# Optimization experiments

Measured on AMD Instinct MI355X. Metric: run time of the kernel, lower is better.

## Reference

```python
import jax, jax.numpy as jnp
import numpy as np

B, S, D = 2, 2048, 1024
E, K = 8, 2
H = 4 * D  # mlp_ratio = 4


def setup_inputs() -> dict:
    key = jax.random.key(0)
    ks = jax.random.split(key, 7)
    s_in = 1.0 / np.sqrt(D)
    s_hid = 1.0 / np.sqrt(H)
    return {
        "x": jax.random.normal(ks[0], (B, S, D), dtype=jnp.float32),
        "w1": jax.random.uniform(ks[1], (E, D, H), jnp.float32, -s_in, s_in),
        "b1": jax.random.uniform(ks[2], (E, H), jnp.float32, -s_in, s_in),
        "w2": jax.random.uniform(ks[3], (E, H, D), jnp.float32, -s_hid, s_hid),
        "b2": jax.random.uniform(ks[4], (E, D), jnp.float32, -s_hid, s_hid),
        "gate_w": jax.random.uniform(ks[5], (D, E), jnp.float32, -s_in, s_in),
        "gate_b": jax.random.uniform(ks[6], (E,), jnp.float32, -s_in, s_in),
    }


def reference(x, w1, b1, w2, b2, gate_w, gate_b):
    # Gating: top-k over expert logits, softmax over the selected k scores.
    scores = jnp.einsum("bsd,de->bse", x, gate_w) + gate_b          # [B,S,E]
    topk_scores, topk_idx = jax.lax.top_k(scores, K)                 # [B,S,K]
    probs = jax.nn.softmax(topk_scores, axis=-1)                     # [B,S,K]

    # Dense per-expert MLP on all tokens (faithful to the original's math).
    h = jnp.einsum("bsd,edh->bseh", x, w1) + b1                      # [B,S,E,H]
    h = jax.nn.gelu(h, approximate=False)                            # torch nn.GELU is exact erf
    y = jnp.einsum("bseh,ehd->bsed", h, w2) + b2                     # [B,S,E,D]

    # Select the top-k expert outputs and combine with softmax weights.
    sel = jnp.take_along_axis(y, topk_idx[..., None], axis=2)        # [B,S,K,D]
    out = jnp.einsum("bsk,bskd->bsd", probs, sel)                    # [B,S,D]
    return out
```

## Files before the change

### kernel.cpp

```cpp
#include <hip/hip_runtime.h>
#include <hip/hip_bf16.h>
#include <stdint.h>

#define D_DIM 1024
#define H_DIM 4096
#define E_NUM 8
#define NTOK  4096
#define CAP_E 4096
#define BM 128
#define BN 128
#define BK 64

typedef __bf16 bf16x8 __attribute__((ext_vector_type(8)));
typedef float  f32x4  __attribute__((ext_vector_type(4)));

static __device__ __forceinline__ unsigned short f2bf(float f) {
    union { float f; unsigned u; } v; v.f = f;
    unsigned r = v.u + 0x7fffu + ((v.u >> 16) & 1u);
    return (unsigned short)(r >> 16);
}

static __device__ __forceinline__ void gload16(const unsigned short* g, unsigned short* l) {
    __builtin_amdgcn_global_load_lds(
        (const __attribute__((address_space(1))) unsigned int*)g,
        (__attribute__((address_space(3))) unsigned int*)l,
        16, 0, 0);
}

static __device__ __forceinline__ float gelu_f(float v) {
    const float z = fabsf(v) * 0.70710678118654752f;
    const float t = __builtin_amdgcn_rcpf(__builtin_fmaf(0.3275911f, z, 1.f));
    float p = __builtin_fmaf(1.061405429f, t, -1.453152027f);
    p = __builtin_fmaf(p, t, 1.421413741f);
    p = __builtin_fmaf(p, t, -0.284496736f);
    p = __builtin_fmaf(p, t, 0.254829592f);
    const float e = 1.f - p * t * __expf(-z * z);
    const float erfv = (v < 0.f) ? -e : e;
    return v * (0.5f + 0.5f * erfv);
}

__global__ __launch_bounds__(256) void gate_kernel(
    const float* __restrict__ x, const float* __restrict__ gw,
    const float* __restrict__ gb, int* __restrict__ counts,
    int* __restrict__ tok_list, float* __restrict__ prob_list,
    unsigned short* __restrict__ xb)
{
    const int wave = threadIdx.x >> 6, lane = threadIdx.x & 63;
    const int t = blockIdx.x * 4 + wave;
    double s[E_NUM];
#pragma unroll
    for (int j = 0; j < E_NUM; ++j) s[j] = 0.0;
    const float* xr = x + (size_t)t * D_DIM;
    unsigned short* xbr = xb + (size_t)t * D_DIM;
#pragma unroll
    for (int i = 0; i < D_DIM / 64; ++i) {
        const int d = i * 64 + lane;
        const float xv = xr[d];
        xbr[d] = f2bf(xv);
        const float4 g0 = *(const float4*)(gw + d * 8);
        const float4 g1 = *(const float4*)(gw + d * 8 + 4);
        s[0] += (double)xv * g0.x; s[1] += (double)xv * g0.y;
        s[2] += (double)xv * g0.z; s[3] += (double)xv * g0.w;
        s[4] += (double)xv * g1.x; s[5] += (double)xv * g1.y;
        s[6] += (double)xv * g1.z; s[7] += (double)xv * g1.w;
    }
#pragma unroll
    for (int off = 32; off >= 1; off >>= 1)
#pragma unroll
        for (int j = 0; j < E_NUM; ++j) s[j] += __shfl_xor(s[j], off, 64);

    if (lane == 0) {
#pragma unroll
        for (int j = 0; j < E_NUM; ++j) s[j] += (double)gb[j];
        int i0 = 0;
        for (int j = 1; j < E_NUM; ++j) if (s[j] > s[i0]) i0 = j;
        int i1 = (i0 == 0) ? 1 : 0;
        for (int j = 0; j < E_NUM; ++j) if (j != i0 && s[j] > s[i1]) i1 = j;
        const double e1 = exp(s[i1] - s[i0]);
        const float p0 = (float)(1.0 / (1.0 + e1));
        const float p1 = (float)(e1 / (1.0 + e1));
        int pos0 = atomicAdd(&counts[i0], 1);
        tok_list[i0 * CAP_E + pos0]  = t;
        prob_list[i0 * CAP_E + pos0] = p0;
        int pos1 = atomicAdd(&counts[i1], 1);
        tok_list[i1 * CAP_E + pos1]  = t;
        prob_list[i1 * CAP_E + pos1] = p1;
    }
}

__global__ void offsets_kernel(const int* __restrict__ counts, int* __restrict__ offsets) {
    if (threadIdx.x == 0) {
        int acc = 0;
        for (int e = 0; e < E_NUM; ++e) { offsets[e] = acc; acc += counts[e]; }
    }
}

__global__ __launch_bounds__(256) void wtrans_kernel(
    const float* __restrict__ in, unsigned short* __restrict__ out, int R, int C)
{
    __shared__ unsigned tile[64][33];
    const size_t slab = (size_t)blockIdx.z * (size_t)R * C;
    const float* inp = in + slab;
    unsigned short* outp = out + slab;
    const int c0 = blockIdx.x * 64, r0 = blockIdx.y * 64;
    const int tid = threadIdx.x;
    const int cq = tid & 15, p0 = tid >> 4;
#pragma unroll
    for (int s = 0; s < 2; ++s) {
        const int p = p0 + s * 16;
        const int r = r0 + 2 * p;
        const int c = c0 + cq * 4;
        const float4 va = *(const float4*)(inp + (size_t)r * C + c);
        const float4 vb = *(const float4*)(inp + (size_t)(r + 1) * C + c);
        const float* fa = (const float*)&va;
        const float* fb = (const float*)&vb;
#pragma unroll
        for (int i = 0; i < 4; ++i)
            tile[cq * 4 + i][p] = (unsigned)f2bf(fa[i]) | ((unsigned)f2bf(fb[i]) << 16);
    }
    __syncthreads();
    const int cl = tid >> 2, q = tid & 3;
#pragma unroll
    for (int s = 0; s < 2; ++s) {
        const int qq = q + s * 4;
        uint4 wv;
        wv.x = tile[cl][qq * 4 + 0]; wv.y = tile[cl][qq * 4 + 1];
        wv.z = tile[cl][qq * 4 + 2]; wv.w = tile[cl][qq * 4 + 3];
        *(uint4*)(outp + (size_t)(c0 + cl) * R + r0 + qq * 8) = wv;
    }
}

__global__ __launch_bounds__(256) void expert_fc1(
    const unsigned short* __restrict__ xb, const unsigned short* __restrict__ w1t,
    const float* __restrict__ b1, const int* __restrict__ counts,
    const int* __restrict__ offsets, const int* __restrict__ tok_list,
    unsigned short* __restrict__ h_ws,
    int e_param, int we_param, int row_start, int cap, int packed)
{
    __shared__ __align__(16) unsigned short smem[12288];
    unsigned short* As = smem;
    unsigned short* Bs = smem + 4096;

    int e, bx, by;
    if (e_param >= 0) { e = e_param; bx = (int)blockIdx.x & 31; by = (int)blockIdx.x >> 5; }
    else { e = (int)blockIdx.x & 7; const int r = (int)blockIdx.x >> 3; bx = r & 31; by = r >> 5; }

    const int we = (we_param >= 0) ? we_param : e;
    const int cnt = counts[e];
    const int row_end = min(cnt, row_start + cap);
    const int row0 = row_start + by * 64;
    if (row0 >= row_end) return;
    const int n0 = bx * BN;
    const int hb = packed ? offsets[e] : 0;
    const int tid = threadIdx.x;

    const int wv = tid >> 6, lane = tid & 63;
    const int schunk = (lane & 7) ^ (lane >> 3);
    const unsigned short* __restrict__ w1e = w1t + (size_t)we * H_DIM * D_DIM;

    const unsigned short* aptr[2];
#pragma unroll
    for (int j = 0; j < 2; ++j) {
        const int rloc = (wv * 2 + j) * 8 + (lane >> 3);
        const int rr = min(row0 + rloc, row_end - 1);
        aptr[j] = xb + (size_t)tok_list[e * CAP_E + rr] * D_DIM + schunk * 8;
    }
    const unsigned short* bptr[4];
#pragma unroll
    for (int j = 0; j < 4; ++j) {
        const int rloc = (wv * 4 + j) * 8 + (lane >> 3);
        bptr[j] = w1e + (size_t)(n0 + rloc) * D_DIM + schunk * 8;
    }

    const int wc = wv * 32;
    const int rl = lane & 15, x7 = lane & 7, kg = lane >> 4;
    int aoff[2][4], boff[2][2];
#pragma unroll
    for (int s = 0; s < 2; ++s) {
        const int slot = ((((s << 2) + kg) ^ x7) << 3);
#pragma unroll
        for (int m = 0; m < 4; ++m) aoff[s][m] = ((m * 16 + rl) << 6) + slot;
#pragma unroll
        for (int n = 0; n < 2; ++n) boff[s][n] = ((wc + n * 16 + rl) << 6) + slot;
    }

    f32x4 acc[4][2];
#pragma unroll
    for (int m = 0; m < 4; ++m)
#pragma unroll
        for (int n = 0; n < 2; ++n) acc[m][n] = (f32x4){0.f, 0.f, 0.f, 0.f};

    for (int kk = 0; kk < D_DIM; kk += BK) {
        __syncthreads();
#pragma unroll
        for (int j = 0; j < 2; ++j)
            gload16(aptr[j] + kk, &As[(wv * 2 + j) * 512]);
#pragma unroll
        for (int j = 0; j < 4; ++j)
            gload16(bptr[j] + kk, &Bs[(wv * 4 + j) * 512]);
        __syncthreads();
#pragma unroll
        for (int s = 0; s < 2; ++s) {
            bf16x8 af[4], bfv[2];
#pragma unroll
            for (int m = 0; m < 4; ++m) af[m] = *(const bf16x8*)&As[aoff[s][m]];
#pragma unroll
            for (int n = 0; n < 2; ++n) bfv[n] = *(const bf16x8*)&Bs[boff[s][n]];
#pragma unroll
            for (int m = 0; m < 4; ++m)
#pragma unroll
                for (int n = 0; n < 2; ++n)
                    acc[m][n] = __builtin_amdgcn_mfma_f32_16x16x32_bf16(af[m], bfv[n], acc[m][n], 0, 0, 0);
        }
    }

    const float* __restrict__ b1e = b1 + e * H_DIM;
    const int crb = (lane >> 4) * 4, ccol = lane & 15;
    float bias[2];
#pragma unroll
    for (int n = 0; n < 2; ++n) bias[n] = b1e[n0 + wc + n * 16 + ccol];

    __syncthreads();
#pragma unroll
    for (int n = 0; n < 2; ++n)
#pragma unroll
        for (int m = 0; m < 4; ++m)
#pragma unroll
            for (int j = 0; j < 4; ++j) {
                const int rloc = m * 16 + crb + j;
                const int col = wc + n * 16 + ccol;
                smem[rloc * 132 + col] = f2bf(gelu_f(acc[m][n][j] + bias[n]));
            }
    __syncthreads();
#pragma unroll
    for (int i = 0; i < 4; ++i) {
        const int idx = tid + i * 256;
        const int row = idx >> 4, c8 = idx & 15;
        const uint4 val = *(const uint4*)&smem[row * 132 + c8 * 8];
        const int gr = row0 + row;
        if (gr < row_end)
            *(uint4*)&h_ws[(size_t)(hb + gr - row_start) * H_DIM + n0 + c8 * 8] = val;
    }
}

__global__ __launch_bounds__(256) void expert_fc2(
    const unsigned short* __restrict__ h_ws, const unsigned short* __restrict__ w2t,
    const float* __restrict__ b2, const int* __restrict__ counts,
    const int* __restrict__ offsets, const int* __restrict__ tok_list,
    const float* __restrict__ prob_list, float* __restrict__ out,
    int splitk, int e_param, int we_param, int row_start, int cap, int packed)
{
    __shared__ __align__(16) unsigned short As[64 * BK];
    __shared__ __align__(16) unsigned short Bs[128 * BK];

    int e, bx, by, ks;
    if (e_param >= 0) { e = e_param; bx = (int)blockIdx.x & 7; by = (int)blockIdx.x >> 3; ks = 0; }
    else { bx = (int)blockIdx.x & 7; int r = (int)blockIdx.x >> 3;
           by = r & 63; r >>= 6; ks = r & 1; e = r >> 1; }

    const int we = (we_param >= 0) ? we_param : e;
    const int cnt = counts[e];
    const int row_end = min(cnt, row_start + cap);
    const int row0 = row_start + by * 64;
    if (row0 >= row_end) return;
    const int n0 = bx * BN;
    const int hb = packed ? offsets[e] : 0;
    const int tid = threadIdx.x;

    const int kspan = H_DIM / splitk;
    const int k0 = ks * kspan;

    const int wv = tid >> 6, lane = tid & 63;
    const int schunk = (lane & 7) ^ (lane >> 3);
    const unsigned short* __restrict__ w2e = w2t + (size_t)we * D_DIM * H_DIM;

    const unsigned short* aptr[2];
#pragma unroll
    for (int j = 0; j < 2; ++j) {
        const int rloc = (wv * 2 + j) * 8 + (lane >> 3);
        int r = row0 + rloc; if (r >= row_end) r = row_end - 1;
        aptr[j] = h_ws + (size_t)(hb + r - row_start) * H_DIM + k0 + schunk * 8;
    }
    const unsigned short* bptr[4];
#pragma unroll
    for (int j = 0; j < 4; ++j) {
        const int rloc = (wv * 4 + j) * 8 + (lane >> 3);
        bptr[j] = w2e + (size_t)(n0 + rloc) * H_DIM + k0 + schunk * 8;
    }

    const int wc = wv * 32;
    const int rl = lane & 15, x7 = lane & 7, kg = lane >> 4;
    int aoff[2][4], boff[2][2];
#pragma unroll
    for (int s = 0; s < 2; ++s) {
        const int slot = ((((s << 2) + kg) ^ x7) << 3);
#pragma unroll
        for (int m = 0; m < 4; ++m) aoff[s][m] = ((m * 16 + rl) << 6) + slot;
#pragma unroll
        for (int n = 0; n < 2; ++n) boff[s][n] = ((wc + n * 16 + rl) << 6) + slot;
    }

    f32x4 acc[4][2];
#pragma unroll
    for (int m = 0; m < 4; ++m)
#pragma unroll
        for (int n = 0; n < 2; ++n) acc[m][n] = (f32x4){0.f, 0.f, 0.f, 0.f};

    for (int kk = 0; kk < kspan; kk += BK) {
        __syncthreads();
#pragma unroll
        for (int j = 0; j < 2; ++j)
            gload16(aptr[j] + kk, &As[(wv * 2 + j) * 512]);
#pragma unroll
        for (int j = 0; j < 4; ++j)
            gload16(bptr[j] + kk, &Bs[(wv * 4 + j) * 512]);
        __syncthreads();
#pragma unroll
        for (int s = 0; s < 2; ++s) {
            bf16x8 af[4], bfv[2];
#pragma unroll
            for (int m = 0; m < 4; ++m) af[m] = *(const bf16x8*)&As[aoff[s][m]];
#pragma unroll
            for (int n = 0; n < 2; ++n) bfv[n] = *(const bf16x8*)&Bs[boff[s][n]];
#pragma unroll
            for (int m = 0; m < 4; ++m)
#pragma unroll
                for (int n = 0; n < 2; ++n)
                    acc[m][n] = __builtin_amdgcn_mfma_f32_16x16x32_bf16(af[m], bfv[n], acc[m][n], 0, 0, 0);
        }
    }

    const float* __restrict__ b2e = b2 + e * D_DIM;
    const int crb = (lane >> 4) * 4, ccol = lane & 15;
#pragma unroll
    for (int n = 0; n < 2; ++n) {
        const int gc = n0 + wc + n * 16 + ccol;
        const float bias = (ks == 0) ? b2e[gc] : 0.f;
#pragma unroll
        for (int m = 0; m < 4; ++m) {
#pragma unroll
            for (int j = 0; j < 4; ++j) {
                const int gr = row0 + m * 16 + crb + j;
                if (gr < row_end) {
                    const float yv = acc[m][n][j] + bias;
                    const int t = tok_list[e * CAP_E + gr];
                    const float p = prob_list[e * CAP_E + gr];
                    atomicAdd(&out[(size_t)t * D_DIM + gc], p * yv);
                }
            }
        }
    }
}

extern "C" void kernel_launch(void* const* d_in, const int* in_sizes, int n_in,
                              void* d_out, int out_size, void* d_ws, size_t ws_size,
                              hipStream_t stream)
{
    const float* x  = (const float*)d_in[0];
    const float* w1 = (const float*)d_in[1];
    const float* b1 = (const float*)d_in[2];
    const float* w2 = (const float*)d_in[3];
    const float* b2 = (const float*)d_in[4];
    const float* gw = (const float*)d_in[5];
    const float* gb = (const float*)d_in[6];
    float* out = (float*)d_out;

    char* w = (char*)d_ws;
    int*   counts    = (int*)w;
    int*   offsets   = (int*)(w + 64);
    int*   tok_list  = (int*)(w + 128);
    float* prob_list = (float*)(w + 128 + (size_t)CAP_E * E_NUM * 4);
    size_t off = 128 + 2 * (size_t)CAP_E * E_NUM * 4;
    off = (off + 255) & ~(size_t)255;
    unsigned short* xb = (unsigned short*)(w + off);
    off += (size_t)NTOK * D_DIM * 2;

    const size_t wslab = (size_t)D_DIM * H_DIM * 2;
    const size_t hfull = (size_t)2 * NTOK * H_DIM * 2;
    const size_t need_full = off + 2 * E_NUM * wslab + hfull;

    hipMemsetAsync(d_out, 0, (size_t)out_size * sizeof(float), stream);
    hipMemsetAsync(counts, 0, 64, stream);

    gate_kernel<<<NTOK / 4, 256, 0, stream>>>(x, gw, gb, counts, tok_list, prob_list, xb);
    offsets_kernel<<<1, 64, 0, stream>>>(counts, offsets);

    if (ws_size >= need_full) {
        unsigned short* w1t = (unsigned short*)(w + off);
        unsigned short* w2t = (unsigned short*)(w + off + E_NUM * wslab);
        unsigned short* h_ws = (unsigned short*)(w + off + 2 * E_NUM * wslab);

        wtrans_kernel<<<dim3(H_DIM / 64, D_DIM / 64, E_NUM), 256, 0, stream>>>(w1, w1t, D_DIM, H_DIM);
        wtrans_kernel<<<dim3(D_DIM / 64, H_DIM / 64, E_NUM), 256, 0, stream>>>(w2, w2t, H_DIM, D_DIM);

        expert_fc1<<<8 * 32 * 64, 256, 0, stream>>>(
            xb, w1t, b1, counts, offsets, tok_list, h_ws, -1, -1, 0, NTOK, 1);
        expert_fc2<<<8 * 64 * 2 * 8, 256, 0, stream>>>(
            h_ws, w2t, b2, counts, offsets, tok_list, prob_list, out,
            2, -1, -1, 0, NTOK, 1);
    } else {
        unsigned short* w1te = (unsigned short*)(w + off);
        unsigned short* w2te = (unsigned short*)(w + off + wslab);
        size_t h_off = off + 2 * wslab;
        unsigned short* h_e = (unsigned short*)(w + h_off);
        size_t h_avail = (ws_size > h_off) ? (ws_size - h_off) / ((size_t)H_DIM * 2) : 0;
        int cap = (int)((h_avail < (size_t)NTOK) ? h_avail : (size_t)NTOK);
        cap = (cap / BM) * BM;
        if (cap < BM) cap = BM;
        const int chunks = (NTOK + cap - 1) / cap;
        for (int e = 0; e < E_NUM; ++e) {
            wtrans_kernel<<<dim3(H_DIM / 64, D_DIM / 64, 1), 256, 0, stream>>>(
                w1 + (size_t)e * D_DIM * H_DIM, w1te, D_DIM, H_DIM);
            wtrans_kernel<<<dim3(D_DIM / 64, H_DIM / 64, 1), 256, 0, stream>>>(
                w2 + (size_t)e * H_DIM * D_DIM, w2te, H_DIM, D_DIM);
            for (int c = 0; c < chunks; ++c) {
                const int rs = c * cap;
                expert_fc1<<<32 * ((cap + 63) / 64), 256, 0, stream>>>(
                    xb, w1te, b1, counts, offsets, tok_list, h_e,
                    e, 0, rs, cap, 0);
                expert_fc2<<<8 * ((cap + 63) / 64), 256, 0, stream>>>(
                    h_e, w2te, b2, counts, offsets, tok_list, prob_list, out,
                    1, e, 0, rs, cap, 0);
            }
        }
    }
}
```

Before: 469.9 us.

## Fuse gate with w1 transpose and fc1 with w2 transpose into combined launches

Merges the gating kernel with the w1 fp32-to-bf16 transpose, and the fc1 GEMM with the w2 transpose, into two combined launches that split work by block index. The memory-bound transpose blocks can then overlap with compute-bound or latency-bound work, and two kernel launch boundaries and their tail effects go away. The cost is a shared LDS pool sized for the largest role, which may reduce occupancy for the transpose blocks, and blocks with mixed behaviour inside one grid.

After: 450.6 us. -4.1%, faster.

```diff
diff --git a/kernel.cpp b/kernel.cpp
--- a/kernel.cpp
+++ b/kernel.cpp
@@ -10,6 +10,11 @@
 #define BM 128
 #define BN 128
 #define BK 64
+
+#define GATE_BLKS (NTOK / 4)
+#define W1T_BLKS  (64 * 16 * E_NUM)
+#define FC1_BLKS  (E_NUM * 32 * 64)
+#define W2T_BLKS  (16 * 64 * E_NUM)
 
 typedef __bf16 bf16x8 __attribute__((ext_vector_type(8)));
 typedef float  f32x4  __attribute__((ext_vector_type(4)));
@@ -39,14 +44,15 @@
     return v * (0.5f + 0.5f * erfv);
 }
 
-__global__ __launch_bounds__(256) void gate_kernel(
+
+static __device__ void gate_body(
     const float* __restrict__ x, const float* __restrict__ gw,
     const float* __restrict__ gb, int* __restrict__ counts,
     int* __restrict__ tok_list, float* __restrict__ prob_list,
-    unsigned short* __restrict__ xb)
+    unsigned short* __restrict__ xb, int bid)
 {
     const int wave = threadIdx.x >> 6, lane = threadIdx.x & 63;
-    const int t = blockIdx.x * 4 + wave;
+    const int t = bid * 4 + wave;
     double s[E_NUM];
 #pragma unroll
     for (int j = 0; j < E_NUM; ++j) s[j] = 0.0;
@@ -88,21 +94,15 @@
     }
 }
 
-__global__ void offsets_kernel(const int* __restrict__ counts, int* __restrict__ offsets) {
-    if (threadIdx.x == 0) {
-        int acc = 0;
-        for (int e = 0; e < E_NUM; ++e) { offsets[e] = acc; acc += counts[e]; }
-    }
-}
-
-__global__ __launch_bounds__(256) void wtrans_kernel(
-    const float* __restrict__ in, unsigned short* __restrict__ out, int R, int C)
-{
-    __shared__ unsigned tile[64][33];
-    const size_t slab = (size_t)blockIdx.z * (size_t)R * C;
+static __device__ void wtrans_body(
+    char* pool, const float* __restrict__ in, unsigned short* __restrict__ out,
+    int R, int C, int cx, int cy, int bz)
+{
+    unsigned (*tile)[33] = (unsigned (*)[33])pool;
+    const size_t slab = (size_t)bz * (size_t)R * C;
     const float* inp = in + slab;
     unsigned short* outp = out + slab;
-    const int c0 = blockIdx.x * 64, r0 = blockIdx.y * 64;
+    const int c0 = cx * 64, r0 = cy * 64;
     const int tid = threadIdx.x;
     const int cq = tid & 15, p0 = tid >> 4;
 #pragma unroll
@@ -130,22 +130,18 @@
     }
 }
 
-__global__ __launch_bounds__(256) void expert_fc1(
+static __device__ void fc1_body(
+    char* pool,
     const unsigned short* __restrict__ xb, const unsigned short* __restrict__ w1t,
     const float* __restrict__ b1, const int* __restrict__ counts,
     const int* __restrict__ offsets, const int* __restrict__ tok_list,
     unsigned short* __restrict__ h_ws,
-    int e_param, int we_param, int row_start, int cap, int packed)
-{
-    __shared__ __align__(16) unsigned short smem[12288];
+    int e, int we, int bx, int by, int row_start, int cap, int packed)
+{
+    unsigned short* smem = (unsigned short*)pool;
     unsigned short* As = smem;
     unsigned short* Bs = smem + 4096;
 
-    int e, bx, by;
-    if (e_param >= 0) { e = e_param; bx = (int)blockIdx.x & 31; by = (int)blockIdx.x >> 5; }
-    else { e = (int)blockIdx.x & 7; const int r = (int)blockIdx.x >> 3; bx = r & 31; by = r >> 5; }
-
-    const int we = (we_param >= 0) ? we_param : e;
     const int cnt = counts[e];
     const int row_end = min(cnt, row_start + cap);
     const int row0 = row_start + by * 64;
@@ -241,6 +237,83 @@
         if (gr < row_end)
             *(uint4*)&h_ws[(size_t)(hb + gr - row_start) * H_DIM + n0 + c8 * 8] = val;
     }
+}
+
+
+__global__ __launch_bounds__(256) void fused_gate_w1trans(
+    const float* __restrict__ x, const float* __restrict__ gw,
+    const float* __restrict__ gb, int* __restrict__ counts,
+    int* __restrict__ tok_list, float* __restrict__ prob_list,
+    unsigned short* __restrict__ xb,
+    const float* __restrict__ w1, unsigned short* __restrict__ w1t)
+{
+    __shared__ __align__(16) char pool[8448];
+    const int bid = (int)blockIdx.x;
+    if (bid < GATE_BLKS) {
+        gate_body(x, gw, gb, counts, tok_list, prob_list, xb, bid);
+    } else {
+        int i = bid - GATE_BLKS;
+        const int cx = i & 63; i >>= 6;
+        const int cy = i & 15; i >>= 4;
+        wtrans_body(pool, w1, w1t, D_DIM, H_DIM, cx, cy, i);
+    }
+}
+
+__global__ __launch_bounds__(256) void gate_kernel(
+    const float* __restrict__ x, const float* __restrict__ gw,
+    const float* __restrict__ gb, int* __restrict__ counts,
+    int* __restrict__ tok_list, float* __restrict__ prob_list,
+    unsigned short* __restrict__ xb)
+{
+    gate_body(x, gw, gb, counts, tok_list, prob_list, xb, (int)blockIdx.x);
+}
+
+__global__ void offsets_kernel(const int* __restrict__ counts, int* __restrict__ offsets) {
+    if (threadIdx.x == 0) {
+        int acc = 0;
+        for (int e = 0; e < E_NUM; ++e) { offsets[e] = acc; acc += counts[e]; }
+    }
+}
+
+__global__ __launch_bounds__(256) void wtrans_kernel(
+    const float* __restrict__ in, unsigned short* __restrict__ out, int R, int C)
+{
+    __shared__ __align__(16) char pool[8448];
+    wtrans_body(pool, in, out, R, C, (int)blockIdx.x, (int)blockIdx.y, (int)blockIdx.z);
+}
+
+__global__ __launch_bounds__(256) void fused_fc1_w2trans(
+    const unsigned short* __restrict__ xb, const unsigned short* __restrict__ w1t,
+    const float* __restrict__ b1, const int* __restrict__ counts,
+    const int* __restrict__ offsets, const int* __restrict__ tok_list,
+    unsigned short* __restrict__ h_ws,
+    const float* __restrict__ w2, unsigned short* __restrict__ w2t)
+{
+    __shared__ __align__(16) char pool[24576];
+    const int bid = (int)blockIdx.x;
+    if (bid < FC1_BLKS) {
+        const int e = bid & 7; const int r = bid >> 3;
+        fc1_body(pool, xb, w1t, b1, counts, offsets, tok_list, h_ws,
+                 e, e, r & 31, r >> 5, 0, NTOK, 1);
+    } else {
+        int i = bid - FC1_BLKS;
+        const int cx = i & 15; i >>= 4;
+        const int cy = i & 63; i >>= 6;
+        wtrans_body(pool, w2, w2t, H_DIM, D_DIM, cx, cy, i);
+    }
+}
+
+__global__ __launch_bounds__(256) void expert_fc1(
+    const unsigned short* __restrict__ xb, const unsigned short* __restrict__ w1t,
+    const float* __restrict__ b1, const int* __restrict__ counts,
+    const int* __restrict__ offsets, const int* __restrict__ tok_list,
+    unsigned short* __restrict__ h_ws,
+    int e_param, int we_param, int row_start, int cap, int packed)
+{
+    __shared__ __align__(16) char pool[24576];
+    const int bx = (int)blockIdx.x & 31, by = (int)blockIdx.x >> 5;
+    fc1_body(pool, xb, w1t, b1, counts, offsets, tok_list, h_ws,
+             e_param, we_param, bx, by, row_start, cap, packed);
 }
 
 __global__ __launch_bounds__(256) void expert_fc2(
@@ -382,23 +455,22 @@
     hipMemsetAsync(d_out, 0, (size_t)out_size * sizeof(float), stream);
     hipMemsetAsync(counts, 0, 64, stream);
 
-    gate_kernel<<<NTOK / 4, 256, 0, stream>>>(x, gw, gb, counts, tok_list, prob_list, xb);
-    offsets_kernel<<<1, 64, 0, stream>>>(counts, offsets);
-
     if (ws_size >= need_full) {
         unsigned short* w1t = (unsigned short*)(w + off);
         unsigned short* w2t = (unsigned short*)(w + off + E_NUM * wslab);
         unsigned short* h_ws = (unsigned short*)(w + off + 2 * E_NUM * wslab);
 
-        wtrans_kernel<<<dim3(H_DIM / 64, D_DIM / 64, E_NUM), 256, 0, stream>>>(w1, w1t, D_DIM, H_DIM);
-        wtrans_kernel<<<dim3(D_DIM / 64, H_DIM / 64, E_NUM), 256, 0, stream>>>(w2, w2t, H_DIM, D_DIM);
-
-        expert_fc1<<<8 * 32 * 64, 256, 0, stream>>>(
-            xb, w1t, b1, counts, offsets, tok_list, h_ws, -1, -1, 0, NTOK, 1);
+        fused_gate_w1trans<<<GATE_BLKS + W1T_BLKS, 256, 0, stream>>>(
+            x, gw, gb, counts, tok_list, prob_list, xb, w1, w1t);
+        offsets_kernel<<<1, 64, 0, stream>>>(counts, offsets);
+        fused_fc1_w2trans<<<FC1_BLKS + W2T_BLKS, 256, 0, stream>>>(
+            xb, w1t, b1, counts, offsets, tok_list, h_ws, w2, w2t);
         expert_fc2<<<8 * 64 * 2 * 8, 256, 0, stream>>>(
             h_ws, w2t, b2, counts, offsets, tok_list, prob_list, out,
             2, -1, -1, 0, NTOK, 1);
     } else {
+        gate_kernel<<<GATE_BLKS, 256, 0, stream>>>(x, gw, gb, counts, tok_list, prob_list, xb);
+        offsets_kernel<<<1, 64, 0, stream>>>(counts, offsets);
         unsigned short* w1te = (unsigned short*)(w + off);
         unsigned short* w2te = (unsigned short*)(w + off + wslab);
         size_t h_off = off + 2 * wslab;
```
